# Performance work log

Measured on AMD Instinct MI355X. Metric: run time of the kernel, lower is better.

Reference implementation:

```python
import jax, jax.numpy as jnp
import numpy as np
from jax import lax

FEAT = 256      # feat_channels
GROUPS = 32     # GN num_groups
NCLS = 80       # num_classes - 1
NRAYS = 36      # polar mask rays
STACK = 4       # stacked_convs
SIZES = [(160, 256), (80, 128), (40, 64), (20, 32), (10, 16)]
B = 1


def conv(x, w, b=None):
    # 3x3 conv, stride 1, pad 1 (SAME). x: [N,C,H,W], w: [O,I,3,3]
    y = lax.conv_general_dilated(x, w, (1, 1), 'SAME',
                                 dimension_numbers=('NCHW', 'OIHW', 'NCHW'))
    if b is not None:
        y = y + b[None, :, None, None]
    return y


def group_norm(x, g, b, eps=1e-5):
    N, C, H, W = x.shape
    xr = x.reshape(N, GROUPS, C // GROUPS, H, W)
    m = xr.mean(axis=(2, 3, 4), keepdims=True)
    v = xr.var(axis=(2, 3, 4), keepdims=True)
    xr = (xr - m) * jax.lax.rsqrt(v + eps)
    return xr.reshape(N, C, H, W) * g[None, :, None, None] + b[None, :, None, None]


def tower(x, ws, gs, bs):
    # ConvModule: conv (no bias, norm present) -> GN -> ReLU, repeated STACK times
    for i in range(STACK):
        x = jax.nn.relu(group_norm(conv(x, ws[i]), gs[i], bs[i]))
    return x


def setup_inputs() -> dict:
    key = jax.random.key(0)
    ks = jax.random.split(key, 32)
    d = {}
    for l, (h, w) in enumerate(SIZES):
        d[f'feat{l}'] = jax.random.normal(ks[l], (B, FEAT, h, w), dtype=jnp.float32)
    std = 0.01
    for j, name in enumerate(['cls', 'reg', 'msk']):
        d[f'{name}_w'] = jax.random.normal(ks[5 + j], (STACK, FEAT, FEAT, 3, 3), jnp.float32) * std
        d[f'{name}_g'] = jnp.ones((STACK, FEAT), jnp.float32)
        d[f'{name}_b'] = jnp.zeros((STACK, FEAT), jnp.float32)
    bias_cls = float(-np.log((1 - 0.01) / 0.01))  # bias_init_with_prob(0.01)
    d['pcls_w'] = jax.random.normal(ks[10], (NCLS, FEAT, 3, 3), jnp.float32) * std
    d['pcls_b'] = jnp.full((NCLS,), bias_cls, jnp.float32)
    d['preg_w'] = jax.random.normal(ks[11], (4, FEAT, 3, 3), jnp.float32) * std
    d['preg_b'] = jnp.zeros((4,), jnp.float32)
    d['pmsk_w'] = jax.random.normal(ks[12], (NRAYS, FEAT, 3, 3), jnp.float32) * std
    d['pmsk_b'] = jnp.zeros((NRAYS,), jnp.float32)
    d['pctr_w'] = jax.random.normal(ks[13], (1, FEAT, 3, 3), jnp.float32) * std
    d['pctr_b'] = jnp.zeros((1,), jnp.float32)
    d['scales_bbox'] = jnp.ones((5,), jnp.float32)
    d['scales_mask'] = jnp.ones((5,), jnp.float32)
    return d


def reference(feat0, feat1, feat2, feat3, feat4,
              cls_w, cls_g, cls_b, reg_w, reg_g, reg_b, msk_w, msk_g, msk_b,
              pcls_w, pcls_b, preg_w, preg_b, pmsk_w, pmsk_b, pctr_w, pctr_b,
              scales_bbox, scales_mask):
    feats = [feat0, feat1, feat2, feat3, feat4]
    cls_outs, bbox_outs, ctr_outs, mask_outs = [], [], [], []
    for l, x in enumerate(feats):
        cf = tower(x, cls_w, cls_g, cls_b)
        cls_outs.append(conv(cf, pcls_w, pcls_b))
        ctr_outs.append(conv(cf, pctr_w, pctr_b))
        rf = tower(x, reg_w, reg_g, reg_b)
        bbox_outs.append(jnp.exp(conv(rf, preg_w, preg_b) * scales_bbox[l]))
        mf = tower(x, msk_w, msk_g, msk_b)
        mask_outs.append(jnp.exp(conv(mf, pmsk_w, pmsk_b) * scales_mask[l]))
    # multi_apply grouping: (cls_scores, bbox_preds, centernesses, mask_preds)
    return tuple(cls_outs) + tuple(bbox_outs) + tuple(ctr_outs) + tuple(mask_outs)
```

## Files before the change

kernel.cpp:

```cpp
#include <hip/hip_runtime.h>

typedef unsigned short u16;
typedef unsigned int u32;
typedef short bf16x8 __attribute__((ext_vector_type(8)));
typedef float f32x4 __attribute__((ext_vector_type(4)));

__device__ __forceinline__ float bf2f(u16 u) {
  u32 x = ((u32)u) << 16;
  float f;
  __builtin_memcpy(&f, &x, 4);
  return f;
}
__device__ __forceinline__ u16 f2bf(float f) {
  u32 x;
  __builtin_memcpy(&x, &f, 4);
  u32 r = x + 0x7FFFu + ((x >> 16) & 1u);
  return (u16)(r >> 16);
}
__device__ __forceinline__ u32 pack2(float f0, float f1) {
  u32 a, b;
  __builtin_memcpy(&a, &f0, 4);
  __builtin_memcpy(&b, &f1, 4);
  a += 0x8000u;
  b += 0x8000u;
  return __builtin_amdgcn_perm(b, a, 0x07060302);
}
__device__ __forceinline__ u32 cvtpk(float f0, float f1) {
  u32 r;
  asm("v_cvt_pk_bf16_f32 %0, %1, %2" : "=v"(r) : "v"(f0), "v"(f1));
  return r;
}
__device__ __forceinline__ void lds_barrier() {
  asm volatile("s_waitcnt lgkmcnt(0)" ::: "memory");
  __builtin_amdgcn_s_barrier();
}


__global__ void convert_weights(const float* __restrict__ cw, const float* __restrict__ rw,
                                const float* __restrict__ mw, const float* __restrict__ pc,
                                const float* __restrict__ pr, const float* __restrict__ pm,
                                const float* __restrict__ pt, u16* __restrict__ dst) {
  int e = blockIdx.x * 256 + threadIdx.x;
  if (e >= 7446528) return;
  float v = 0.f;
  if (e < 7077888) {
    int conv = e / 589824, r = e % 589824;
    int mo = r / 294912;
    int r2 = r - mo * 294912;
    int kt = r2 >> 12;
    int r3 = r2 & 4095;
    int wm = r3 >> 11;
    int mi = (r3 >> 9) & 3;
    int l = (r3 >> 3) & 63;
    int j = r3 & 7;
    int ch = kt / 9, ti = kt - ch * 9;
    int dxs = ti / 3, dys = ti - dxs * 3;
    int tap = dys * 3 + dxs;
    int o = mo * 128 + wm * 64 + mi * 16 + (l & 15);
    int c = ch * 32 + (l >> 4) * 8 + j;
    const float* s = (conv < 4) ? cw : (conv < 8) ? rw : mw;
    int si = conv & 3;
    v = s[((si * 256 + o) * 256 + c) * 9 + tap];
  } else {
    int e2 = e - 7077888;
    int kt, r2, mi, mtsel;
    const float* src = nullptr;
    int olim = 0;
    bool ctr = false;
    if (e2 < 221184) {
      kt = e2 / 3072; r2 = e2 % 3072; mi = r2 / 512; r2 %= 512;
      src = pc; olim = 80; ctr = true;
    } else if (e2 < 258048) {
      int e3 = e2 - 221184;
      kt = e3 / 512; r2 = e3 % 512; mi = 0;
      src = pr; olim = 4;
    } else {
      int e3 = e2 - 258048;
      kt = e3 / 1536; r2 = e3 % 1536; mi = r2 / 512; r2 %= 512;
      src = pm; olim = 36;
    }
    int l = r2 >> 3, j = r2 & 7;
    int ch = kt / 9, ti = kt - ch * 9;
    int dxs = ti / 3, dys = ti - dxs * 3;
    int tap = dys * 3 + dxs;
    int o = mi * 16 + (l & 15);
    int c = ch * 32 + (l >> 4) * 8 + j;
    if (o < olim) v = src[(o * 256 + c) * 9 + tap];
    else if (ctr && o == 80) v = pt[c * 9 + tap];
    (void)mtsel;
  }
  dst[e] = f2bf(v);
}

__global__ void halo_zero(u16* __restrict__ X, u16* __restrict__ Y, long ACT, int ntw) {
  int i = blockIdx.x * 256 + threadIdx.x;
  int rep = i / 26112;
  int j = i - rep * 26112;
  if (rep >= 2 * ntw) return;
  int hp = j >> 4, sub = j & 15;
  int Wp, Hp, pxb, h;
  if (hp < 836)       { Wp = 258; Hp = 162; pxb = 0;     h = hp; }
  else if (hp < 1256) { Wp = 130; Hp = 82;  pxb = 41796; h = hp - 836; }
  else if (hp < 1468) { Wp = 66;  Hp = 42;  pxb = 52456; h = hp - 1256; }
  else if (hp < 1576) { Wp = 34;  Hp = 22;  pxb = 55228; h = hp - 1468; }
  else                { Wp = 18;  Hp = 12;  pxb = 55976; h = hp - 1576; }
  int y, x;
  if (h < Wp)          { y = 0;      x = h; }
  else if (h < 2 * Wp) { y = Hp - 1; x = h - Wp; }
  else {
    int rr = h - 2 * Wp;
    y = 1 + (rr >> 1);
    x = (rr & 1) ? (Wp - 1) : 0;
  }
  u16* buf = (rep < ntw) ? (X + rep * ACT) : (Y + (rep - ntw) * ACT);
  long adr = (long)(pxb + y * Wp + x) * 256 + sub * 16;
  uint4 z = {0, 0, 0, 0};
  *(uint4*)(buf + adr) = z;
  *(uint4*)(buf + adr + 8) = z;
}

__global__ void feat_to_nhwc(const float* __restrict__ f0, const float* __restrict__ f1,
                             const float* __restrict__ f2, const float* __restrict__ f3,
                             const float* __restrict__ f4, u16* __restrict__ dst,
                             long tstride, int nrep) {
  __shared__ float lds[64 * 65];
  int bx = blockIdx.x;
  int tile = bx >> 2, c0 = (bx & 3) * 64;
  int tl, sh, pxb, npx;
  const float* src;
  if (tile < 640)      { tl = tile;       sh = 8; pxb = 0;     npx = 40960; src = f0; }
  else if (tile < 800) { tl = tile - 640; sh = 7; pxb = 41796; npx = 10240; src = f1; }
  else if (tile < 840) { tl = tile - 800; sh = 6; pxb = 52456; npx = 2560;  src = f2; }
  else if (tile < 850) { tl = tile - 840; sh = 5; pxb = 55228; npx = 640;   src = f3; }
  else                 { tl = tile - 850; sh = 4; pxb = 55976; npx = 160;   src = f4; }
  int W = 1 << sh, Wp = W + 2;
  int px0 = tl * 64;
  int t = threadIdx.x;
  {
    int cc = (t >> 6) * 16, px = t & 63;
    bool ok = (px0 + px) < npx;
#pragma unroll
    for (int j = 0; j < 16; ++j) {
      float v = ok ? src[(c0 + cc + j) * npx + px0 + px] : 0.f;
      lds[(cc + j) * 65 + px] = v;
    }
  }
  __syncthreads();
  {
    int px = t >> 2, cL = (t & 3) * 16;
    int pxi = px0 + px;
    if (pxi < npx) {
      int y = pxi >> sh, x = pxi & (W - 1);
      u32 w[8];
#pragma unroll
      for (int j = 0; j < 8; ++j)
        w[j] = pack2(lds[(cL + 2 * j) * 65 + px], lds[(cL + 2 * j + 1) * 65 + px]);
      long adr = (long)(pxb + (y + 1) * Wp + (x + 1)) * 256 + c0 + cL;
      uint4 v0 = {w[0], w[1], w[2], w[3]}, v1 = {w[4], w[5], w[6], w[7]};
      for (int r = 0; r < nrep; ++r) {
        *(uint4*)(dst + r * tstride + adr) = v0;
        *(uint4*)(dst + r * tstride + adr + 8) = v1;
      }
    }
  }
}

__global__ void finalize_stats(const float* __restrict__ stats, int st_ts,
                               const float* __restrict__ g0, const float* __restrict__ g1,
                               const float* __restrict__ g2, const float* __restrict__ b0,
                               const float* __restrict__ b1, const float* __restrict__ b2,
                               float* __restrict__ scaleb, int sb_ts, int ntw) {
  int i = blockIdx.x * 256 + threadIdx.x;
  if (i >= ntw * 1280) return;
  int tw = i / 1280, r = i - tw * 1280, lvl = r >> 8, c = r & 255, g = c >> 3;
  float cnt = (lvl == 0) ? 327680.f : (lvl == 1) ? 81920.f
              : (lvl == 2) ? 20480.f : (lvl == 3) ? 5120.f : 1280.f;
  float s1 = stats[tw * st_ts + (lvl * 32 + g) * 2];
  float s2 = stats[tw * st_ts + (lvl * 32 + g) * 2 + 1];
  float mean = s1 / cnt;
  float var = s2 / cnt - mean * mean;
  float inv = rsqrtf(fmaxf(var, 0.f) + 1e-5f);
  const float* ga = (tw == 0) ? g0 : (tw == 1) ? g1 : g2;
  const float* be = (tw == 0) ? b0 : (tw == 1) ? b1 : b2;
  float sc = inv * ga[c];
  scaleb[(long)tw * sb_ts + (lvl * 256 + c) * 2] = sc;
  scaleb[(long)tw * sb_ts + (lvl * 256 + c) * 2 + 1] = be[c] - mean * sc;
}

__global__ __launch_bounds__(256, 3) void conv_tower(
    const u16* __restrict__ Xn, long in_ts, const u16* __restrict__ Wt, long wt_ts,
    u16* __restrict__ Yraw, long out_ts, float* __restrict__ stats, int st_ts,
    const float* __restrict__ scaleb, int sb_ts, int do_gn) {
  __shared__ __align__(16) u16 Btile[11520];
  __shared__ float shSB[512];
  __shared__ float sred[32];
  int bx = blockIdx.x;
  int tw = bx / 856, r856 = bx - tw * 856;
  Xn += tw * in_ts; Wt += tw * wt_ts; Yraw += tw * out_ts; stats += tw * st_ts;
  int tile = r856 >> 1, mo = r856 & 1;
  int tloc, W, H, SX, pxb, lvl;
  if (tile < 320)      { lvl = 0; tloc = tile;       W = 256; H = 160; SX = 4; pxb = 0; }
  else if (tile < 400) { lvl = 1; tloc = tile - 320; W = 128; H = 80;  SX = 3; pxb = 41796; }
  else if (tile < 420) { lvl = 2; tloc = tile - 400; W = 64;  H = 40;  SX = 2; pxb = 52456; }
  else if (tile < 426) { lvl = 3; tloc = tile - 420; W = 32;  H = 20;  SX = 1; pxb = 55228; }
  else                 { lvl = 4; tloc = tile - 426; W = 16;  H = 10;  SX = 0; pxb = 55976; }
  int Wp = W + 2;
  int ty = tloc >> SX, txi = tloc & ((1 << SX) - 1);
  int y0 = ty * 8, x0 = txi * 16;
  int t = threadIdx.x, lane = t & 63, wave = t >> 6;
  int wm = wave >> 1, wn = wave & 1;
  int quad = lane >> 4, col = lane & 15;
  const u16* Xbase = Xn + (long)(pxb + y0 * Wp + x0) * 256;
  const u16* Wb = Wt + (long)mo * 294912 + wm * 2048 + (long)lane * 8;
  int bcol = quad * 1440 + wn * 576 + col * 8;
  if (do_gn) {
    float2 sv = *(const float2*)(scaleb + (long)tw * sb_ts + (lvl * 256 + t) * 2);
    *(float2*)(&shSB[t * 2]) = sv;
  }
  const u16* Pptr[3];
  int Lo[3], Cb[3];
  bool Uok[3], Keep[3];
#pragma unroll
  for (int i = 0; i < 3; ++i) {
    int u = t + i * 256;
    Uok[i] = u < 720;
    int q = u & 3, p = u >> 2;
    int py = p / 18, px = p - py * 18;
    Pptr[i] = Xbase + (long)(py * Wp + px) * 256 + q * 8;
    Lo[i] = q * 1440 + p * 8;
    Cb[i] = q * 8;
    int yg = y0 + py, xg = x0 + px;
    Keep[i] = (yg >= 1) && (yg <= H) && (xg >= 1) && (xg <= W);
  }
  uint4 breg[3];
#pragma unroll
  for (int i = 0; i < 3; ++i)
    if (Uok[i]) breg[i] = *(const uint4*)(Pptr[i]);
  bf16x8 areg[3][4];
#pragma unroll
  for (int mi = 0; mi < 4; ++mi) areg[0][mi] = *(const bf16x8*)(Wb + mi * 512);
#pragma unroll
  for (int mi = 0; mi < 4; ++mi) areg[1][mi] = *(const bf16x8*)(Wb + 4096 + mi * 512);
  f32x4 acc[4][4] = {};
  auto stage = [&](int bo, int cc) {
#pragma unroll
    for (int i = 0; i < 3; ++i) {
      if (Uok[i]) {
        uint4 v = breg[i];
        if (do_gn) {
          int cb2 = (Cb[i] + cc * 32) * 2;
          float4 s01 = *(const float4*)(&shSB[cb2]);
          float4 s23 = *(const float4*)(&shSB[cb2 + 4]);
          float4 s45 = *(const float4*)(&shSB[cb2 + 8]);
          float4 s67 = *(const float4*)(&shSB[cb2 + 12]);
          u32 wv[4] = {v.x, v.y, v.z, v.w};
          float sc[8] = {s01.x, s01.z, s23.x, s23.z, s45.x, s45.z, s67.x, s67.z};
          float bi[8] = {s01.y, s01.w, s23.y, s23.w, s45.y, s45.w, s67.y, s67.w};
          bool kp = Keep[i];
          u32 ow[4];
#pragma unroll
          for (int jj = 0; jj < 4; ++jj) {
            u32 lo32 = wv[jj] << 16, hi32 = wv[jj] & 0xffff0000u;
            float flo, fhi;
            __builtin_memcpy(&flo, &lo32, 4);
            __builtin_memcpy(&fhi, &hi32, 4);
            float f0 = fmaxf(flo * sc[2 * jj] + bi[2 * jj], 0.f);
            float f1 = fmaxf(fhi * sc[2 * jj + 1] + bi[2 * jj + 1], 0.f);
            ow[jj] = cvtpk(f0, f1);
          }
          v.x = kp ? ow[0] : 0u;
          v.y = kp ? ow[1] : 0u;
          v.z = kp ? ow[2] : 0u;
          v.w = kp ? ow[3] : 0u;
        }
        *(uint4*)(Btile + bo + Lo[i]) = v;
      }
    }
  };
  __syncthreads();
  stage(0, 0);
#pragma unroll
  for (int i = 0; i < 3; ++i)
    if (Uok[i]) breg[i] = *(const uint4*)(Pptr[i] + 32);
  __syncthreads();
  for (int ch = 0; ch < 8; ++ch) {
    int bb = (ch & 1) * 5760;
    if (ch < 7) stage(5760 - bb, ch + 1);
    bf16x8 brow[6];
#pragma unroll
    for (int ti = 0; ti < 9; ++ti) {
      int kt = ch * 9 + ti;
      int dxq = ti / 3, dyq = ti - dxq * 3;
      if (dyq == 0) {
#pragma unroll
        for (int r = 0; r < 6; ++r)
          brow[r] = *(const bf16x8*)(Btile + bb + bcol + r * 144 + dxq * 8);
      }
      {
        const u16* wn_ = Wb + (long)(kt + 2) * 4096;
#pragma unroll
        for (int mi = 0; mi < 4; ++mi)
          areg[(ti + 2) % 3][mi] = *(const bf16x8*)(wn_ + mi * 512);
      }
      if (ti == 0 && ch < 6) {
#pragma unroll
        for (int i = 0; i < 3; ++i)
          if (Uok[i]) breg[i] = *(const uint4*)(Pptr[i] + (ch + 2) * 32);
      }
      __builtin_amdgcn_s_setprio(1);
#pragma unroll
      for (int ni = 0; ni < 4; ++ni) {
        bf16x8 b = brow[dyq + ni];
#pragma unroll
        for (int mi = 0; mi < 4; ++mi)
          acc[mi][ni] =
              __builtin_amdgcn_mfma_f32_16x16x32_bf16(areg[ti % 3][mi], b, acc[mi][ni], 0, 0, 0);
      }
      __builtin_amdgcn_s_setprio(0);
    }
    lds_barrier();
  }
  if (t < 32) sred[t] = 0.f;
  __syncthreads();
  long pebase = (long)(pxb + (y0 + 1) * Wp + (x0 + col + 1)) * 256;
#pragma unroll
  for (int ni = 0; ni < 4; ++ni) {
    int row = wn * 4 + ni;
    if (y0 + row < H) {
#pragma unroll
      for (int mi = 0; mi < 4; ++mi) {
        f32x4 v = acc[mi][ni];
        int o = mo * 128 + wm * 64 + mi * 16 + quad * 4;
        uint2 pk;
        pk.x = cvtpk(v[0], v[1]);
        pk.y = cvtpk(v[2], v[3]);
        *(uint2*)(Yraw + pebase + (long)row * Wp * 256 + o) = pk;
      }
    }
  }
#pragma unroll
  for (int mi = 0; mi < 4; ++mi) {
    float s1 = 0.f, s2 = 0.f;
#pragma unroll
    for (int ni = 0; ni < 4; ++ni) {
      if (y0 + wn * 4 + ni < H) {
        f32x4 v = acc[mi][ni];
#pragma unroll
        for (int r2 = 0; r2 < 4; ++r2) { float f = v[r2]; s1 += f; s2 += f * f; }
      }
    }
#pragma unroll
    for (int m = 1; m < 16; m <<= 1) { s1 += __shfl_xor(s1, m); s2 += __shfl_xor(s2, m); }
    if (col == 0) {
      int g = (wm * 64 + mi * 16 + quad * 4) >> 3;
      atomicAdd(&sred[g * 2], s1);
      atomicAdd(&sred[g * 2 + 1], s2);
    }
  }
  __syncthreads();
  if (t < 32) atomicAdd(&stats[(lvl * 32 + mo * 16 + (t >> 1)) * 2 + (t & 1)], sred[t]);
}

__global__ __launch_bounds__(256, 3) void conv_head_fused(
    const u16* __restrict__ Xbase, long ACT, int htsel, const u16* __restrict__ Whead,
    float* __restrict__ out, const float* __restrict__ pcb, const float* __restrict__ ptb,
    const float* __restrict__ prb, const float* __restrict__ pmb,
    const float* __restrict__ sb, const float* __restrict__ sm,
    const float* __restrict__ scaleb, long sb_ts) {
  __shared__ __align__(16) u16 Btile[11520];
  __shared__ float shSB[512];
  int bx = blockIdx.x;
  int ht, r;
  if (htsel >= 0) { ht = htsel; r = bx; }
  else { ht = bx / 428; r = bx - ht * 428; }
  int MI, woff, mt32;
  const float* bias0;
  const float* scl;
  if (ht == 0)      { MI = 6; woff = 0;      mt32 = 3072; bias0 = pcb; scl = sb; }
  else if (ht == 1) { MI = 1; woff = 221184; mt32 = 512;  bias0 = prb; scl = sb; }
  else              { MI = 3; woff = 258048; mt32 = 1536; bias0 = pmb; scl = sm; }
  const u16* Xn = Xbase + ((htsel >= 0) ? 0 : (long)ht * ACT);
  int tloc, W, H, SX, pxb, lvl, npx;
  if (r < 320)      { lvl = 0; tloc = r;       W = 256; H = 160; SX = 4; pxb = 0;     npx = 40960; }
  else if (r < 400) { lvl = 1; tloc = r - 320; W = 128; H = 80;  SX = 3; pxb = 41796; npx = 10240; }
  else if (r < 420) { lvl = 2; tloc = r - 400; W = 64;  H = 40;  SX = 2; pxb = 52456; npx = 2560;  }
  else if (r < 426) { lvl = 3; tloc = r - 420; W = 32;  H = 20;  SX = 1; pxb = 55228; npx = 640;   }
  else              { lvl = 4; tloc = r - 426; W = 16;  H = 10;  SX = 0; pxb = 55976; npx = 160;   }
  int obm, obc = 0;
  if (ht == 0) {
    const int obms[5] = {0, 3276800, 4096000, 4300800, 4352000};
    const int obcs[5] = {4583040, 4624000, 4634240, 4636800, 4637440};
    obm = obms[lvl]; obc = obcs[lvl];
  } else if (ht == 1) {
    const int obms[5] = {4364800, 4528640, 4569600, 4579840, 4582400};
    obm = obms[lvl];
  } else {
    const int obms[5] = {4637600, 6112160, 6480800, 6572960, 6596000};
    obm = obms[lvl];
  }
  int Wp = W + 2;
  int ty = tloc >> SX, txi = tloc & ((1 << SX) - 1);
  int y0 = ty * 8, x0 = txi * 16;
  int t = threadIdx.x, lane = t & 63, wave = t >> 6;
  int quad = lane >> 4, col = lane & 15;
  const u16* Xb2 = Xn + (long)(pxb + y0 * Wp + x0) * 256;
  const u16* Wb = Whead + woff + (long)lane * 8;
  {
    float2 sv = *(const float2*)(scaleb + ht * sb_ts + (lvl * 256 + t) * 2);
    *(float2*)(&shSB[t * 2]) = sv;
  }
  const u16* Pptr[3];
  int Lo[3], Cb[3];
  bool Uok[3], Keep[3];
#pragma unroll
  for (int i = 0; i < 3; ++i) {
    int u = t + i * 256;
    Uok[i] = u < 720;
    int q = u & 3, p = u >> 2;
    int py = p / 18, px = p - py * 18;
    Pptr[i] = Xb2 + (long)(py * Wp + px) * 256 + q * 8;
    Lo[i] = q * 1440 + p * 8;
    Cb[i] = q * 8;
    int yg = y0 + py, xg = x0 + px;
    Keep[i] = (yg >= 1) && (yg <= H) && (xg >= 1) && (xg <= W);
  }
  uint4 breg[3];
#pragma unroll
  for (int i = 0; i < 3; ++i)
    if (Uok[i]) breg[i] = *(const uint4*)(Pptr[i]);
  bf16x8 areg[2][6];
#pragma unroll
  for (int mi = 0; mi < 6; ++mi)
    if (mi < MI) areg[0][mi] = *(const bf16x8*)(Wb + mi * 512);
  f32x4 acc[6][2] = {};
  int brbase = quad * 1440 + wave * 288 + col * 8;
  auto stage = [&](int bo, int cc) {
#pragma unroll
    for (int i = 0; i < 3; ++i) {
      if (Uok[i]) {
        uint4 v = breg[i];
        int cb2 = (Cb[i] + cc * 32) * 2;
        float4 s01 = *(const float4*)(&shSB[cb2]);
        float4 s23 = *(const float4*)(&shSB[cb2 + 4]);
        float4 s45 = *(const float4*)(&shSB[cb2 + 8]);
        float4 s67 = *(const float4*)(&shSB[cb2 + 12]);
        u32 wv[4] = {v.x, v.y, v.z, v.w};
        float sc[8] = {s01.x, s01.z, s23.x, s23.z, s45.x, s45.z, s67.x, s67.z};
        float bi[8] = {s01.y, s01.w, s23.y, s23.w, s45.y, s45.w, s67.y, s67.w};
        bool kp = Keep[i];
        u32 ow[4];
#pragma unroll
        for (int jj = 0; jj < 4; ++jj) {
          u32 lo32 = wv[jj] << 16, hi32 = wv[jj] & 0xffff0000u;
          float flo, fhi;
          __builtin_memcpy(&flo, &lo32, 4);
          __builtin_memcpy(&fhi, &hi32, 4);
          float f0 = fmaxf(flo * sc[2 * jj] + bi[2 * jj], 0.f);
          float f1 = fmaxf(fhi * sc[2 * jj + 1] + bi[2 * jj + 1], 0.f);
          ow[jj] = cvtpk(f0, f1);
        }
        v.x = kp ? ow[0] : 0u;
        v.y = kp ? ow[1] : 0u;
        v.z = kp ? ow[2] : 0u;
        v.w = kp ? ow[3] : 0u;
        *(uint4*)(Btile + bo + Lo[i]) = v;
      }
    }
  };
  __syncthreads();
  stage(0, 0);
#pragma unroll
  for (int i = 0; i < 3; ++i)
    if (Uok[i]) breg[i] = *(const uint4*)(Pptr[i] + 32);
  __syncthreads();
  for (int ch = 0; ch < 8; ++ch) {
    int bb = (ch & 1) * 5760;
    if (ch < 7) stage(5760 - bb, ch + 1);
    if (ch < 6) {
#pragma unroll
      for (int i = 0; i < 3; ++i)
        if (Uok[i]) breg[i] = *(const uint4*)(Pptr[i] + (ch + 2) * 32);
    }
    bf16x8 brow[4];
#pragma unroll
    for (int ti = 0; ti < 9; ++ti) {
      int kt = ch * 9 + ti;
      int dxq = ti / 3, dyq = ti - dxq * 3;
      if (dyq == 0) {
#pragma unroll
        for (int rr = 0; rr < 4; ++rr)
          brow[rr] = *(const bf16x8*)(Btile + bb + brbase + rr * 144 + dxq * 8);
      }
      {
        const u16* wn_ = Wb + (long)(kt + 1) * mt32;
#pragma unroll
        for (int mi = 0; mi < 6; ++mi)
          if (mi < MI) areg[(ti + 1) & 1][mi] = *(const bf16x8*)(wn_ + mi * 512);
      }
#pragma unroll
      for (int ni = 0; ni < 2; ++ni) {
        bf16x8 b = brow[dyq + ni];
#pragma unroll
        for (int mi = 0; mi < 6; ++mi)
          if (mi < MI)
            acc[mi][ni] =
                __builtin_amdgcn_mfma_f32_16x16x32_bf16(areg[ti & 1][mi], b, acc[mi][ni], 0, 0, 0);
      }
    }
#pragma unroll
    for (int mi = 0; mi < 6; ++mi)
      if (mi < MI) areg[0][mi] = areg[1][mi];
    lds_barrier();
  }
  float scv = scl[lvl];
  int x = x0 + col;
#pragma unroll
  for (int ni = 0; ni < 2; ++ni) {
    int y = y0 + 2 * wave + ni;
    if (y < H) {
#pragma unroll
      for (int mi = 0; mi < 6; ++mi) {
        if (mi < MI) {
#pragma unroll
          for (int r2 = 0; r2 < 4; ++r2) {
            int o = mi * 16 + quad * 4 + r2;
            float v = acc[mi][ni][r2];
            if (ht == 0) {
              if (o < 80) out[obm + o * npx + y * W + x] = v + bias0[o];
              else if (o == 80) out[obc + y * W + x] = v + ptb[0];
            } else if (ht == 1) {
              if (o < 4) out[obm + o * npx + y * W + x] = expf((v + bias0[o]) * scv);
            } else {
              if (o < 36) out[obm + o * npx + y * W + x] = expf((v + bias0[o]) * scv);
            }
          }
        }
      }
    }
  }
}

extern "C" void kernel_launch(void* const* d_in, const int* in_sizes, int n_in,
                              void* d_out, int out_size, void* d_ws, size_t ws_size,
                              hipStream_t stream) {
  const float* feat0 = (const float*)d_in[0];
  const float* feat1 = (const float*)d_in[1];
  const float* feat2 = (const float*)d_in[2];
  const float* feat3 = (const float*)d_in[3];
  const float* feat4 = (const float*)d_in[4];
  const float* cw = (const float*)d_in[5];
  const float* rw = (const float*)d_in[8];
  const float* mw = (const float*)d_in[11];
  const float* gmas[3] = {(const float*)d_in[6], (const float*)d_in[9], (const float*)d_in[12]};
  const float* btas[3] = {(const float*)d_in[7], (const float*)d_in[10], (const float*)d_in[13]};
  const float* pcw = (const float*)d_in[14];
  const float* pcb = (const float*)d_in[15];
  const float* prw = (const float*)d_in[16];
  const float* prb = (const float*)d_in[17];
  const float* pmw = (const float*)d_in[18];
  const float* pmb = (const float*)d_in[19];
  const float* ptw = (const float*)d_in[20];
  const float* ptb = (const float*)d_in[21];
  const float* sb = (const float*)d_in[22];
  const float* sm = (const float*)d_in[23];
  float* out = (float*)d_out;

  const long ACT = 14385152;
  const long ACTB = 28770304;
  const long WTS = 14893056;
  char* base = (char*)d_ws;
  u16* wts = (u16*)base;

  size_t need_fused = WTS + 6 * (size_t)ACTB + 3840 + 30720 + 65536;

  convert_weights<<<29088, 256, 0, stream>>>(cw, rw, mw, pcw, prw, pmw, ptw, wts);

  if (ws_size >= need_fused) {
    u16* X = (u16*)(base + WTS);
    u16* Y = (u16*)(base + WTS + 3 * ACTB);
    float* stats = (float*)(base + WTS + 6 * ACTB);
    float* scaleb = (float*)(base + WTS + 6 * ACTB + 3840);
    halo_zero<<<612, 256, 0, stream>>>(X, Y, ACT, 3);
    feat_to_nhwc<<<3412, 256, 0, stream>>>(feat0, feat1, feat2, feat3, feat4, X, ACT, 1);
    for (int s = 0; s < 4; ++s) {
      u16* in = (s & 1) ? Y : X;
      u16* ot = (s & 1) ? X : Y;
      long ints = (s == 0) ? 0 : ACT;
      hipMemsetAsync(stats, 0, 3840, stream);
      conv_tower<<<2568, 256, 0, stream>>>(in, ints, wts + s * 589824, 4 * 589824, ot, ACT,
                                           stats, 320, scaleb, 2560, s > 0);
      finalize_stats<<<15, 256, 0, stream>>>(stats, 320,
                                             gmas[0] + s * 256, gmas[1] + s * 256, gmas[2] + s * 256,
                                             btas[0] + s * 256, btas[1] + s * 256, btas[2] + s * 256,
                                             scaleb, 2560, 3);
    }
    conv_head_fused<<<1284, 256, 0, stream>>>(X, ACT, -1, wts + 7077888, out,
                                              pcb, ptb, prb, pmb, sb, sm, scaleb, 2560);
  } else {
    u16* bufA = (u16*)(base + WTS);
    u16* bufB = (u16*)(base + WTS + ACTB);
    float* stats = (float*)(base + WTS + 2 * ACTB);
    float* scaleb = (float*)(base + WTS + 2 * ACTB + 1280);
    halo_zero<<<204, 256, 0, stream>>>(bufA, bufB, 0, 1);
    for (int tw = 0; tw < 3; ++tw) {
      feat_to_nhwc<<<3412, 256, 0, stream>>>(feat0, feat1, feat2, feat3, feat4, bufA, 0, 1);
      for (int s = 0; s < 4; ++s) {
        u16* in = (s & 1) ? bufB : bufA;
        u16* ot = (s & 1) ? bufA : bufB;
        hipMemsetAsync(stats, 0, 1280, stream);
        conv_tower<<<856, 256, 0, stream>>>(in, 0, wts + (tw * 4 + s) * 589824, 0, ot, 0,
                                            stats, 0, scaleb, 0, s > 0);
        finalize_stats<<<5, 256, 0, stream>>>(stats, 0,
                                              gmas[tw] + s * 256, gmas[tw] + s * 256, gmas[tw] + s * 256,
                                              btas[tw] + s * 256, btas[tw] + s * 256, btas[tw] + s * 256,
                                              scaleb, 0, 1);
      }
      conv_head_fused<<<428, 256, 0, stream>>>(bufA, 0, tw, wts + 7077888, out,
                                               pcb, ptb, prb, pmb, sb, sm, scaleb, 0);
    }
  }
}
```

Measured before the change: 957.6 us.

## Switch tower conv to 32x32x16 MFMA with matching weight layout

Replaces the 16x16x32 bf16 MFMA tiling in the tower conv kernel with 32x32x16 MFMAs: a 2x2 grid of 32x32 accumulators per wave instead of 4x4 of 16x16. The weight pre-conversion layout, LDS B-fragment addressing, epilogue store and GroupNorm statistic reduction are all remapped to the new lane layout. The aim is fewer MFMA issues and fewer LDS/weight fragment loads per FLOP. In exchange the K-loop gets restructured with more weight loads per iteration, and the new output channel mapping could be wrong if any index is off.

```diff
diff --git a/kernel.cpp b/kernel.cpp
--- a/kernel.cpp
+++ b/kernel.cpp
@@ -4,6 +4,7 @@
 typedef unsigned int u32;
 typedef short bf16x8 __attribute__((ext_vector_type(8)));
 typedef float f32x4 __attribute__((ext_vector_type(4)));
+typedef float f32x16 __attribute__((ext_vector_type(16)));
 
 __device__ __forceinline__ float bf2f(u16 u) {
   u32 x = ((u32)u) << 16;
@@ -47,23 +48,26 @@
     int conv = e / 589824, r = e % 589824;
     int mo = r / 294912;
     int r2 = r - mo * 294912;
-    int kt = r2 >> 12;
-    int r3 = r2 & 4095;
-    int wm = r3 >> 11;
-    int mi = (r3 >> 9) & 3;
+    int kt2 = r2 >> 11;
+    int r3 = r2 & 2047;
+    int wm = r3 >> 10;
+    int mi = (r3 >> 9) & 1;
     int l = (r3 >> 3) & 63;
     int j = r3 & 7;
-    int ch = kt / 9, ti = kt - ch * 9;
-    int dxs = ti / 3, dys = ti - dxs * 3;
-    int tap = dys * 3 + dxs;
-    int o = mo * 128 + wm * 64 + mi * 16 + (l & 15);
-    int c = ch * 32 + (l >> 4) * 8 + j;
+    int dy = kt2 % 3;
+    int tq = kt2 / 3;
+    int ks = tq & 1;
+    int t2 = tq >> 1;
+    int dx = t2 % 3, cs = t2 / 3;
+    int tap = dy * 3 + dx;
+    int o = mo * 128 + wm * 64 + mi * 32 + (l & 31);
+    int c = cs * 32 + ks * 16 + (l >> 5) * 8 + j;
     const float* s = (conv < 4) ? cw : (conv < 8) ? rw : mw;
     int si = conv & 3;
     v = s[((si * 256 + o) * 256 + c) * 9 + tap];
   } else {
     int e2 = e - 7077888;
-    int kt, r2, mi, mtsel;
+    int kt, r2, mi;
     const float* src = nullptr;
     int olim = 0;
     bool ctr = false;
@@ -87,7 +91,6 @@
     int c = ch * 32 + (l >> 4) * 8 + j;
     if (o < olim) v = src[(o * 256 + c) * 9 + tap];
     else if (ctr && o == 80) v = pt[c * 9 + tap];
-    (void)mtsel;
   }
   dst[e] = f2bf(v);
 }
@@ -209,10 +212,9 @@
   int y0 = ty * 8, x0 = txi * 16;
   int t = threadIdx.x, lane = t & 63, wave = t >> 6;
   int wm = wave >> 1, wn = wave & 1;
-  int quad = lane >> 4, col = lane & 15;
   const u16* Xbase = Xn + (long)(pxb + y0 * Wp + x0) * 256;
-  const u16* Wb = Wt + (long)mo * 294912 + wm * 2048 + (long)lane * 8;
-  int bcol = quad * 1440 + wn * 576 + col * 8;
+  const u16* Wb = Wt + (long)mo * 294912 + wm * 1024 + (long)lane * 8;
+  int lnB = (lane >> 5) * 1440 + ((lane >> 4) & 1) * 144 + (lane & 15) * 8;
   if (do_gn) {
     float2 sv = *(const float2*)(scaleb + (long)tw * sb_ts + (lvl * 256 + t) * 2);
     *(float2*)(&shSB[t * 2]) = sv;
@@ -236,12 +238,12 @@
 #pragma unroll
   for (int i = 0; i < 3; ++i)
     if (Uok[i]) breg[i] = *(const uint4*)(Pptr[i]);
-  bf16x8 areg[3][4];
-#pragma unroll
-  for (int mi = 0; mi < 4; ++mi) areg[0][mi] = *(const bf16x8*)(Wb + mi * 512);
-#pragma unroll
-  for (int mi = 0; mi < 4; ++mi) areg[1][mi] = *(const bf16x8*)(Wb + 4096 + mi * 512);
-  f32x4 acc[4][4] = {};
+  bf16x8 areg[3][2];
+#pragma unroll
+  for (int mi = 0; mi < 2; ++mi) areg[0][mi] = *(const bf16x8*)(Wb + mi * 512);
+#pragma unroll
+  for (int mi = 0; mi < 2; ++mi) areg[1][mi] = *(const bf16x8*)(Wb + 2048 + mi * 512);
+  f32x16 acc[2][2] = {};
   auto stage = [&](int bo, int cc) {
 #pragma unroll
     for (int i = 0; i < 3; ++i) {
@@ -286,75 +288,87 @@
   for (int ch = 0; ch < 8; ++ch) {
     int bb = (ch & 1) * 5760;
     if (ch < 7) stage(5760 - bb, ch + 1);
-    bf16x8 brow[6];
-#pragma unroll
-    for (int ti = 0; ti < 9; ++ti) {
-      int kt = ch * 9 + ti;
-      int dxq = ti / 3, dyq = ti - dxq * 3;
-      if (dyq == 0) {
-#pragma unroll
-        for (int r = 0; r < 6; ++r)
-          brow[r] = *(const bf16x8*)(Btile + bb + bcol + r * 144 + dxq * 8);
-      }
-      {
-        const u16* wn_ = Wb + (long)(kt + 2) * 4096;
-#pragma unroll
-        for (int mi = 0; mi < 4; ++mi)
-          areg[(ti + 2) % 3][mi] = *(const bf16x8*)(wn_ + mi * 512);
-      }
-      if (ti == 0 && ch < 6) {
-#pragma unroll
-        for (int i = 0; i < 3; ++i)
-          if (Uok[i]) breg[i] = *(const uint4*)(Pptr[i] + (ch + 2) * 32);
-      }
-      __builtin_amdgcn_s_setprio(1);
-#pragma unroll
-      for (int ni = 0; ni < 4; ++ni) {
-        bf16x8 b = brow[dyq + ni];
-#pragma unroll
-        for (int mi = 0; mi < 4; ++mi)
-          acc[mi][ni] =
-              __builtin_amdgcn_mfma_f32_16x16x32_bf16(areg[ti % 3][mi], b, acc[mi][ni], 0, 0, 0);
-      }
-      __builtin_amdgcn_s_setprio(0);
+#pragma unroll
+    for (int dx = 0; dx < 3; ++dx) {
+#pragma unroll
+      for (int ks = 0; ks < 2; ++ks) {
+        bf16x8 brow2[5];
+#pragma unroll
+        for (int yb = 0; yb < 5; ++yb)
+          brow2[yb] =
+              *(const bf16x8*)(Btile + bb + ks * 2880 + (wn * 4 + yb) * 144 + dx * 8 + lnB);
+#pragma unroll
+        for (int dy = 0; dy < 3; ++dy) {
+          int idx = (dx * 2 + ks) * 3 + dy;
+          int kt2 = ch * 18 + idx;
+          {
+            const u16* wn_ = Wb + (long)(kt2 + 2) * 2048;
+#pragma unroll
+            for (int mi = 0; mi < 2; ++mi)
+              areg[(dy + 2) % 3][mi] = *(const bf16x8*)(wn_ + mi * 512);
+          }
+          if (idx == 0 && ch < 6) {
+#pragma unroll
+            for (int i = 0; i < 3; ++i)
+              if (Uok[i]) breg[i] = *(const uint4*)(Pptr[i] + (ch + 2) * 32);
+          }
+          __builtin_amdgcn_s_setprio(1);
+#pragma unroll
+          for (int ni = 0; ni < 2; ++ni) {
+            bf16x8 b = brow2[ni * 2 + dy];
+#pragma unroll
+            for (int mi = 0; mi < 2; ++mi)
+              acc[mi][ni] = __builtin_amdgcn_mfma_f32_32x32x16_bf16(areg[dy][mi], b,
+                                                                    acc[mi][ni], 0, 0, 0);
+          }
+          __builtin_amdgcn_s_setprio(0);
+        }
+      }
     }
     lds_barrier();
   }
   if (t < 32) sred[t] = 0.f;
   __syncthreads();
-  long pebase = (long)(pxb + (y0 + 1) * Wp + (x0 + col + 1)) * 256;
-#pragma unroll
-  for (int ni = 0; ni < 4; ++ni) {
-    int row = wn * 4 + ni;
-    if (y0 + row < H) {
-#pragma unroll
-      for (int mi = 0; mi < 4; ++mi) {
-        f32x4 v = acc[mi][ni];
-        int o = mo * 128 + wm * 64 + mi * 16 + quad * 4;
-        uint2 pk;
-        pk.x = cvtpk(v[0], v[1]);
-        pk.y = cvtpk(v[2], v[3]);
-        *(uint2*)(Yraw + pebase + (long)row * Wp * 256 + o) = pk;
-      }
-    }
-  }
-#pragma unroll
-  for (int mi = 0; mi < 4; ++mi) {
-    float s1 = 0.f, s2 = 0.f;
-#pragma unroll
-    for (int ni = 0; ni < 4; ++ni) {
-      if (y0 + wn * 4 + ni < H) {
-        f32x4 v = acc[mi][ni];
-#pragma unroll
-        for (int r2 = 0; r2 < 4; ++r2) { float f = v[r2]; s1 += f; s2 += f * f; }
-      }
-    }
-#pragma unroll
-    for (int m = 1; m < 16; m <<= 1) { s1 += __shfl_xor(s1, m); s2 += __shfl_xor(s2, m); }
-    if (col == 0) {
-      int g = (wm * 64 + mi * 16 + quad * 4) >> 3;
-      atomicAdd(&sred[g * 2], s1);
-      atomicAdd(&sred[g * 2 + 1], s2);
+  int xl = lane & 15, ysub = (lane >> 4) & 1, lh = lane >> 5;
+#pragma unroll
+  for (int ni = 0; ni < 2; ++ni) {
+    int y = wn * 4 + ni * 2 + ysub;
+    if (y0 + y < H) {
+      long pe = (long)(pxb + (y0 + y + 1) * Wp + (x0 + xl + 1)) * 256;
+#pragma unroll
+      for (int mi = 0; mi < 2; ++mi) {
+        f32x16 v = acc[mi][ni];
+#pragma unroll
+        for (int rq = 0; rq < 4; ++rq) {
+          int o = mo * 128 + wm * 64 + mi * 32 + rq * 8 + lh * 4;
+          uint2 pk;
+          pk.x = cvtpk(v[rq * 4 + 0], v[rq * 4 + 1]);
+          pk.y = cvtpk(v[rq * 4 + 2], v[rq * 4 + 3]);
+          *(uint2*)(Yraw + pe + o) = pk;
+        }
+      }
+    }
+  }
+#pragma unroll
+  for (int mi = 0; mi < 2; ++mi) {
+#pragma unroll
+    for (int rq = 0; rq < 4; ++rq) {
+      float s1 = 0.f, s2 = 0.f;
+#pragma unroll
+      for (int ni = 0; ni < 2; ++ni) {
+        if (y0 + wn * 4 + ni * 2 + ysub < H) {
+          f32x16 v = acc[mi][ni];
+#pragma unroll
+          for (int r2 = 0; r2 < 4; ++r2) { float f = v[rq * 4 + r2]; s1 += f; s2 += f * f; }
+        }
+      }
+#pragma unroll
+      for (int m = 1; m < 32; m <<= 1) { s1 += __shfl_xor(s1, m); s2 += __shfl_xor(s2, m); }
+      if ((lane & 31) == 0) {
+        int g = wm * 8 + mi * 4 + rq;
+        atomicAdd(&sred[g * 2], s1);
+        atomicAdd(&sred[g * 2 + 1], s2);
+      }
     }
   }
   __syncthreads();
```

Measured after the change: 1.081 ms. +12.9%, slower.
